# Kernel tuning notes

Measured on AMD Instinct MI355X. Metric: run time of the kernel, lower is better.

Reference implementation:

```python
import jax, jax.numpy as jnp
import numpy as np

EMB_DIM = 1024
NUM_HEADS = 16
HEAD_DIM = EMB_DIM // NUM_HEADS
B, S = 4, 1024


def _split_heads(x):
    # [B, S, E] -> [B, H, S, E/H]
    b, s, e = x.shape
    return x.reshape(b, s, NUM_HEADS, e // NUM_HEADS).transpose(0, 2, 1, 3)


def _merge_heads(x):
    # [B, H, S, D] -> [B, S, H*D]
    b, h, s, d = x.shape
    return x.transpose(0, 2, 1, 3).reshape(b, s, h * d)


def setup_inputs() -> dict:
    key = jax.random.key(0)
    ks = jax.random.split(key, 8)
    w_scale = 0.02
    return {
        "Re": jax.random.normal(ks[0], (B, S, EMB_DIM), jnp.float32),
        "Im": jax.random.normal(ks[1], (B, S, EMB_DIM), jnp.float32),
        "pos_enc": jax.random.normal(ks[2], (B, S, HEAD_DIM), jnp.float32),
        "Wq": jax.random.normal(ks[3], (EMB_DIM, EMB_DIM), jnp.float32) * w_scale,
        "bq": jnp.zeros((EMB_DIM,), jnp.float32),
        "Wk": jax.random.normal(ks[4], (EMB_DIM, EMB_DIM), jnp.float32) * w_scale,
        "bk": jnp.zeros((EMB_DIM,), jnp.float32),
        "Wv": jax.random.normal(ks[5], (EMB_DIM, EMB_DIM), jnp.float32) * w_scale,
        "bv": jnp.zeros((EMB_DIM,), jnp.float32),
        "Wo": jax.random.normal(ks[6], (EMB_DIM, EMB_DIM), jnp.float32) * w_scale,
        "bo": jnp.zeros((EMB_DIM,), jnp.float32),
    }


def reference(Re, Im, pos_enc, Wq, bq, Wk, bk, Wv, bv, Wo, bo):
    # projections + head split
    Q = _split_heads(Re @ Wq + bq)          # [B,H,S,D]
    K = _split_heads(Re @ Wk + bk)          # [B,H,S,D]
    ImH = _split_heads(Im)                  # [B,H,S,D]
    P = pos_enc[:, None, :, :]              # [B,1,S,D] broadcast over heads
    Q = Q + P
    K = K + P
    # real part of (Q + i*Im)(K - i*Im)^T = Q K^T + Im Im^T
    denom = jnp.sqrt(jnp.asarray(EMB_DIM, Q.dtype))  # NOTE: sqrt(emb_dim), as in source
    scores = (jnp.einsum("bhqd,bhkd->bhqk", Q, K)
              + jnp.einsum("bhqd,bhkd->bhqk", ImH, ImH)) / denom
    weights = jax.nn.softmax(scores, axis=-1)
    V = _split_heads(Re @ Wv + bv) + P      # value_pos_enc=True
    out = jnp.einsum("bhqk,bhkd->bhqd", weights, V)
    return _merge_heads(out) @ Wo + bo
```

## Files before the change

kernel.cpp:

```cpp
#include <hip/hip_runtime.h>
#include <hip/hip_bf16.h>
#include <stdint.h>

#define BATCH 4
#define SEQ   1024
#define EMB   1024
#define NHEAD 16
#define HDIM  64
#define MTOT  (BATCH*SEQ)
#define MELEM (MTOT*EMB)

typedef __attribute__((ext_vector_type(8))) short short8;
typedef __attribute__((ext_vector_type(4))) float f32x4;
typedef __attribute__((ext_vector_type(4))) unsigned short us4;

static __device__ __forceinline__ unsigned short f2bf_fast(float f) {
  unsigned u = __builtin_bit_cast(unsigned, f);
  return (unsigned short)((u + 0x8000u) >> 16);
}

static __device__ __forceinline__ void cp16(const void* g, const void* lds_uniform) {
  __builtin_amdgcn_global_load_lds(
      (const __attribute__((address_space(1))) unsigned int*)(uintptr_t)g,
      (__attribute__((address_space(3))) unsigned int*)(unsigned int)(uintptr_t)lds_uniform,
      16, 0, 0);
}

__global__ __launch_bounds__(256) void cvt_bf16(const float* __restrict__ in0,
                                                const float* __restrict__ in1,
                                                short* __restrict__ out0,
                                                short* __restrict__ out1) {
  const float* in  = blockIdx.y ? in1  : in0;
  short*       out = blockIdx.y ? out1 : out0;
  int i = blockIdx.x * 256 + threadIdx.x;
  float4 f = ((const float4*)in)[i];
  unsigned r0 = ((unsigned)f2bf_fast(f.y) << 16) | f2bf_fast(f.x);
  unsigned r1 = ((unsigned)f2bf_fast(f.w) << 16) | f2bf_fast(f.z);
  ((uint2*)out)[i] = make_uint2(r0, r1);
}

__global__ __launch_bounds__(256) void wtrans(const float* __restrict__ W0,
                                              const float* __restrict__ W1,
                                              const float* __restrict__ W2,
                                              const float* __restrict__ W3,
                                              short* __restrict__ WtBase) {
  const int z = blockIdx.z;
  const float* W = (z == 0) ? W0 : (z == 1) ? W1 : (z == 2) ? W2 : W3;
  short* Wt = WtBase + (size_t)z * EMB * EMB;
  __shared__ short tile[32][33];
  int nT = blockIdx.x * 32, kT = blockIdx.y * 32;
  int tx = threadIdx.x, ty = threadIdx.y;
  #pragma unroll
  for (int i = 0; i < 4; ++i)
    tile[ty + 8*i][tx] = (short)f2bf_fast(W[(size_t)(kT + ty + 8*i) * EMB + nT + tx]);
  __syncthreads();
  #pragma unroll
  for (int i = 0; i < 4; ++i)
    Wt[(size_t)(nT + ty + 8*i) * EMB + kT + tx] = tile[tx][ty + 8*i];
}

__global__ __launch_bounds__(256) void gemm_qkv(const short* __restrict__ A,
                                                const short* __restrict__ Wt,
                                                const float* __restrict__ bq,
                                                const float* __restrict__ bk,
                                                const float* __restrict__ bv,
                                                const float* __restrict__ pos,
                                                short* __restrict__ QKbase,
                                                short* __restrict__ vtOut) {
  const int m0 = blockIdx.y * 128, n0 = blockIdx.x * 64;
  const int z = n0 >> 10;
  const float* bias = (z == 0) ? bq : (z == 1 ? bk : bv);

  __shared__ __align__(16) short As[128 * 64];
  __shared__ __align__(16) short Bs[64 * 64];

  const int t = threadIdx.x;
  const int lane = t & 63, w = t >> 6;
  const int wm = w >> 1, wn = w & 1;
  const int quad = lane >> 4, l16 = lane & 15;
  const int lrow8 = lane >> 3, lchunk = lane & 7;
  const int gch = lchunk ^ lrow8;
  const int sw7 = l16 & 7;

  const short* Arow = A  + (size_t)(m0 + w * 32 + lrow8) * EMB + gch * 8;
  const short* Brow = Wt + (size_t)(n0 + w * 16 + lrow8) * EMB + gch * 8;

  f32x4 acc[4][2] = {};

  for (int k0 = 0; k0 < EMB; k0 += 64) {
    #pragma unroll
    for (int s = 0; s < 4; ++s)
      cp16(Arow + (size_t)(s * 8) * EMB + k0, &As[(w * 32 + s * 8) * 64]);
    #pragma unroll
    for (int s = 0; s < 2; ++s)
      cp16(Brow + (size_t)(s * 8) * EMB + k0, &Bs[(w * 16 + s * 8) * 64]);
    __syncthreads();
    #pragma unroll
    for (int ks = 0; ks < 2; ++ks) {
      const int chv = ((ks << 2) + quad) ^ sw7;
      short8 af[4], bfr[2];
      #pragma unroll
      for (int i = 0; i < 4; ++i)
        af[i] = *(const short8*)&As[(wm * 64 + i * 16 + l16) * 64 + chv * 8];
      #pragma unroll
      for (int j = 0; j < 2; ++j)
        bfr[j] = *(const short8*)&Bs[(wn * 32 + j * 16 + l16) * 64 + chv * 8];
      #pragma unroll
      for (int i = 0; i < 4; ++i)
        #pragma unroll
        for (int j = 0; j < 2; ++j)
          acc[i][j] = __builtin_amdgcn_mfma_f32_16x16x32_bf16(af[i], bfr[j], acc[i][j], 0, 0, 0);
    }
    __syncthreads();
  }

  #pragma unroll
  for (int i = 0; i < 4; ++i) {
    int mbase = m0 + wm * 64 + i * 16 + quad * 4;
    #pragma unroll
    for (int j = 0; j < 2; ++j) {
      int n = n0 + wn * 32 + j * 16 + l16;
      int nl = n & 1023;
      float bn = bias[nl];
      int d = nl & (HDIM - 1);
      if (z == 2) {
        int bh = (mbase >> 10) * NHEAD + (nl >> 6);
        int s = mbase & (SEQ - 1);
        us4 pk;
        #pragma unroll
        for (int r = 0; r < 4; ++r) {
          float v = acc[i][j][r] + bn + pos[(size_t)(mbase + r) * HDIM + d];
          pk[r] = f2bf_fast(v);
        }
        *(us4*)&vtOut[((size_t)bh * HDIM + d) * SEQ + s] = pk;
      } else {
        #pragma unroll
        for (int r = 0; r < 4; ++r) {
          int mm = mbase + r;
          float v = acc[i][j][r] + bn + pos[(size_t)mm * HDIM + d];
          QKbase[(size_t)z * MELEM + (size_t)mm * EMB + nl] = (short)f2bf_fast(v);
        }
      }
    }
  }
}

__global__ __launch_bounds__(256) void gemm_wo(const short* __restrict__ A,
                                               const short* __restrict__ Bt,
                                               const float* __restrict__ bias,
                                               float* __restrict__ out) {
  const int m0 = blockIdx.y * 64, n0 = blockIdx.x * 64;

  __shared__ __align__(16) short As[64 * 64];
  __shared__ __align__(16) short Bs[64 * 64];

  const int t = threadIdx.x;
  const int lane = t & 63, w = t >> 6;
  const int wm = w >> 1, wn = w & 1;
  const int quad = lane >> 4, l16 = lane & 15;
  const int lrow8 = lane >> 3, lchunk = lane & 7;
  const int gch = lchunk ^ lrow8;
  const int sw7 = l16 & 7;

  const short* Arow = A  + (size_t)(m0 + w * 16 + lrow8) * EMB + gch * 8;
  const short* Brow = Bt + (size_t)(n0 + w * 16 + lrow8) * EMB + gch * 8;

  f32x4 acc[2][2] = {};

  for (int k0 = 0; k0 < EMB; k0 += 64) {
    #pragma unroll
    for (int s = 0; s < 2; ++s) {
      cp16(Arow + (size_t)(s * 8) * EMB + k0, &As[(w * 16 + s * 8) * 64]);
      cp16(Brow + (size_t)(s * 8) * EMB + k0, &Bs[(w * 16 + s * 8) * 64]);
    }
    __syncthreads();
    #pragma unroll
    for (int ks = 0; ks < 2; ++ks) {
      const int chv = ((ks << 2) + quad) ^ sw7;
      short8 af[2], bfr[2];
      #pragma unroll
      for (int i = 0; i < 2; ++i)
        af[i] = *(const short8*)&As[(wm * 32 + i * 16 + l16) * 64 + chv * 8];
      #pragma unroll
      for (int j = 0; j < 2; ++j)
        bfr[j] = *(const short8*)&Bs[(wn * 32 + j * 16 + l16) * 64 + chv * 8];
      #pragma unroll
      for (int i = 0; i < 2; ++i)
        #pragma unroll
        for (int j = 0; j < 2; ++j)
          acc[i][j] = __builtin_amdgcn_mfma_f32_16x16x32_bf16(af[i], bfr[j], acc[i][j], 0, 0, 0);
    }
    __syncthreads();
  }

  #pragma unroll
  for (int i = 0; i < 2; ++i) {
    int mbase = m0 + wm * 32 + i * 16 + quad * 4;
    #pragma unroll
    for (int j = 0; j < 2; ++j) {
      int n = n0 + wn * 32 + j * 16 + l16;
      float bn = bias[n];
      #pragma unroll
      for (int r = 0; r < 4; ++r)
        out[(size_t)(mbase + r) * EMB + n] = acc[i][j][r] + bn;
    }
  }
}

__global__ __launch_bounds__(256) void attn(const short* __restrict__ Qp,
                                            const short* __restrict__ Kp,
                                            const short* __restrict__ VtG,
                                            const short* __restrict__ Imb,
                                            short* __restrict__ attnA) {
  const int qb = blockIdx.y * 64;
  const int bh = blockIdx.x;
  const int b = bh >> 4, h = bh & 15;
  const int t = threadIdx.x, lane = t & 63, w = t >> 6;
  const int quad = lane >> 4, l16 = lane & 15;
  const int lrow8 = lane >> 3, lchunk = lane & 7;
  const int gch = lchunk ^ lrow8;
  const int sw7 = l16 & 7;

  __shared__ __align__(16) short tiles[3 * 64 * 64];
  __shared__ __align__(16) short Pw[4 * 16 * 64];

  const int q = qb + w * 16 + l16;
  const size_t qoff = ((size_t)(b * SEQ + q)) * EMB + h * HDIM + quad * 8;
  short8 aq[2], aim[2];
  aq[0]  = *(const short8*)&Qp [qoff];
  aq[1]  = *(const short8*)&Qp [qoff + 32];
  aim[0] = *(const short8*)&Imb[qoff];
  aim[1] = *(const short8*)&Imb[qoff + 32];

  float lr[4] = {0.f, 0.f, 0.f, 0.f};
  f32x4 o[4] = {};

  const float SC = 0.03125f * 1.44269504089f;
  const size_t kimBase = ((size_t)b * SEQ) * EMB + h * HDIM + gch * 8;
  const size_t vtBase  = ((size_t)bh * HDIM) * SEQ + gch * 8;

  #pragma unroll
  for (int s = 0; s < 6; ++s) {
    const int I = w * 6 + s;
    const int tz = I >> 3;
    const int row = ((I & 7) * 8) + lrow8;
    const short* g;
    if (tz == 0)      g = Kp  + kimBase + (size_t)row * EMB;
    else if (tz == 1) g = Imb + kimBase + (size_t)row * EMB;
    else              g = VtG + vtBase + (size_t)row * SEQ;
    cp16(g, &tiles[I * 512]);
  }
  __syncthreads();

  for (int kt = 0; kt < 16; ++kt) {
    const int kBaseN = (kt + 1) * 64;

    f32x4 sa[4] = {};
    #pragma unroll
    for (int c = 0; c < 4; ++c) {
      const int rowoff = (c * 16 + l16) * 64;
      #pragma unroll
      for (int st = 0; st < 2; ++st) {
        const int chv = (((st << 2) + quad) ^ sw7) * 8;
        short8 bk = *(const short8*)&tiles[rowoff + chv];
        short8 bi = *(const short8*)&tiles[4096 + rowoff + chv];
        sa[c] = __builtin_amdgcn_mfma_f32_16x16x32_bf16(aq [st], bk, sa[c], 0, 0, 0);
        sa[c] = __builtin_amdgcn_mfma_f32_16x16x32_bf16(aim[st], bi, sa[c], 0, 0, 0);
      }
    }

    __syncthreads();

    if (kt != 15) {
      #pragma unroll
      for (int s = 0; s < 4; ++s) {
        const int I = w * 4 + s;
        const int row = ((I & 7) * 8) + lrow8;
        const short* g = ((I >> 3) ? Imb : Kp) + kimBase + (size_t)(kBaseN + row) * EMB;
        cp16(g, &tiles[I * 512]);
      }
    }

    short* pw = &Pw[w * 1024];
    #pragma unroll
    for (int c = 0; c < 4; ++c) {
      #pragma unroll
      for (int r = 0; r < 4; ++r) {
        float p = __builtin_amdgcn_exp2f(sa[c][r] * SC);
        lr[r] += p;
        const int row = quad * 4 + r;
        const int sch = ((c * 2 + (l16 >> 3)) ^ (row & 7));
        pw[row * 64 + sch * 8 + (l16 & 7)] = (short)f2bf_fast(p);
      }
    }
    short8 ap[2];
    ap[0] = *(const short8*)&pw[l16 * 64 + ((quad       ^ sw7) * 8)];
    ap[1] = *(const short8*)&pw[l16 * 64 + (((4 + quad) ^ sw7) * 8)];

    #pragma unroll
    for (int cd = 0; cd < 4; ++cd) {
      const int rowoff = 8192 + (cd * 16 + l16) * 64;
      #pragma unroll
      for (int st = 0; st < 2; ++st) {
        short8 bv2 = *(const short8*)&tiles[rowoff + (((st << 2) + quad) ^ sw7) * 8];
        o[cd] = __builtin_amdgcn_mfma_f32_16x16x32_bf16(ap[st], bv2, o[cd], 0, 0, 0);
      }
    }

    __syncthreads();

    if (kt != 15) {
      #pragma unroll
      for (int s = 0; s < 2; ++s) {
        const int I = 16 + w * 2 + s;
        const int row = ((I & 7) * 8) + lrow8;
        cp16(VtG + vtBase + (size_t)row * SEQ + kBaseN, &tiles[I * 512]);
      }
    }
  }

  #pragma unroll
  for (int r = 0; r < 4; ++r) {
    #pragma unroll
    for (int msk = 1; msk < 16; msk <<= 1) lr[r] += __shfl_xor(lr[r], msk);
  }
  #pragma unroll
  for (int r = 0; r < 4; ++r) {
    int qq = qb + w * 16 + quad * 4 + r;
    float inv = 1.f / lr[r];
    size_t base = ((size_t)(b * SEQ + qq)) * EMB + h * HDIM;
    #pragma unroll
    for (int cd = 0; cd < 4; ++cd)
      attnA[base + cd * 16 + l16] = (short)f2bf_fast(o[cd][r] * inv);
  }
}

extern "C" void kernel_launch(void* const* d_in, const int* in_sizes, int n_in,
                              void* d_out, int out_size, void* d_ws, size_t ws_size,
                              hipStream_t stream) {
  const float* Re  = (const float*)d_in[0];
  const float* Im  = (const float*)d_in[1];
  const float* pos = (const float*)d_in[2];
  const float* Wq  = (const float*)d_in[3];
  const float* bq  = (const float*)d_in[4];
  const float* Wk  = (const float*)d_in[5];
  const float* bk  = (const float*)d_in[6];
  const float* Wv  = (const float*)d_in[7];
  const float* bv  = (const float*)d_in[8];
  const float* Wo  = (const float*)d_in[9];
  const float* bo  = (const float*)d_in[10];

  short* ws    = (short*)d_ws;
  short* Rebf  = ws;
  short* Imbf  = ws + (size_t)MELEM;
  short* Wt    = ws + (size_t)2 * MELEM;
  short* Qp    = ws + (size_t)3 * MELEM;
  short* Kp    = Qp + (size_t)MELEM;
  short* VtG   = Qp + (size_t)2 * MELEM;
  short* attnA = ws + (size_t)6 * MELEM;

  cvt_bf16<<<dim3(MELEM / 1024, 2), 256, 0, stream>>>(Re, Im, Rebf, Imbf);

  wtrans<<<dim3(32, 32, 4), dim3(32, 8), 0, stream>>>(Wq, Wk, Wv, Wo, Wt);

  gemm_qkv<<<dim3(3 * EMB / 64, MTOT / 128), 256, 0, stream>>>(
      Rebf, Wt, bq, bk, bv, pos, Qp, VtG);

  attn<<<dim3(BATCH * NHEAD, SEQ / 64), 256, 0, stream>>>(
      Qp, Kp, VtG, Imbf, attnA);

  gemm_wo<<<dim3(EMB / 64, MTOT / 64), 256, 0, stream>>>(
      attnA, Wt + 3 * EMB * EMB, bo, (float*)d_out);
}
```

Baseline: 206.1 us.

## Enlarge output tiles in QKV, Wo and attention kernels for more reuse

Doubles the per-block tile in all three compute kernels: the QKV GEMM goes to 128x128, the Wo GEMM to 128x64, and each attention block handles 128 queries with two 16-row groups per wave. Each K/Im/V tile loaded into LDS now feeds twice as many MFMAs, which cuts global and LDS traffic per FLOP. In exchange, accumulator register pressure rises and grids shrink (attention drops to 512 blocks, QKV to 768), which can hurt occupancy and how evenly blocks spread across CUs.

```diff
diff --git a/kernel.cpp b/kernel.cpp
--- a/kernel.cpp
+++ b/kernel.cpp
@@ -67,12 +67,12 @@
                                                 const float* __restrict__ pos,
                                                 short* __restrict__ QKbase,
                                                 short* __restrict__ vtOut) {
-  const int m0 = blockIdx.y * 128, n0 = blockIdx.x * 64;
+  const int m0 = blockIdx.y * 128, n0 = blockIdx.x * 128;
   const int z = n0 >> 10;
   const float* bias = (z == 0) ? bq : (z == 1 ? bk : bv);
 
   __shared__ __align__(16) short As[128 * 64];
-  __shared__ __align__(16) short Bs[64 * 64];
+  __shared__ __align__(16) short Bs[128 * 64];
 
   const int t = threadIdx.x;
   const int lane = t & 63, w = t >> 6;
@@ -83,32 +83,32 @@
   const int sw7 = l16 & 7;
 
   const short* Arow = A  + (size_t)(m0 + w * 32 + lrow8) * EMB + gch * 8;
-  const short* Brow = Wt + (size_t)(n0 + w * 16 + lrow8) * EMB + gch * 8;
-
-  f32x4 acc[4][2] = {};
+  const short* Brow = Wt + (size_t)(n0 + w * 32 + lrow8) * EMB + gch * 8;
+
+  f32x4 acc[4][4] = {};
 
   for (int k0 = 0; k0 < EMB; k0 += 64) {
     #pragma unroll
     for (int s = 0; s < 4; ++s)
       cp16(Arow + (size_t)(s * 8) * EMB + k0, &As[(w * 32 + s * 8) * 64]);
     #pragma unroll
-    for (int s = 0; s < 2; ++s)
-      cp16(Brow + (size_t)(s * 8) * EMB + k0, &Bs[(w * 16 + s * 8) * 64]);
+    for (int s = 0; s < 4; ++s)
+      cp16(Brow + (size_t)(s * 8) * EMB + k0, &Bs[(w * 32 + s * 8) * 64]);
     __syncthreads();
     #pragma unroll
     for (int ks = 0; ks < 2; ++ks) {
       const int chv = ((ks << 2) + quad) ^ sw7;
-      short8 af[4], bfr[2];
+      short8 af[4], bfr[4];
       #pragma unroll
       for (int i = 0; i < 4; ++i)
         af[i] = *(const short8*)&As[(wm * 64 + i * 16 + l16) * 64 + chv * 8];
       #pragma unroll
-      for (int j = 0; j < 2; ++j)
-        bfr[j] = *(const short8*)&Bs[(wn * 32 + j * 16 + l16) * 64 + chv * 8];
+      for (int j = 0; j < 4; ++j)
+        bfr[j] = *(const short8*)&Bs[(wn * 64 + j * 16 + l16) * 64 + chv * 8];
       #pragma unroll
       for (int i = 0; i < 4; ++i)
         #pragma unroll
-        for (int j = 0; j < 2; ++j)
+        for (int j = 0; j < 4; ++j)
           acc[i][j] = __builtin_amdgcn_mfma_f32_16x16x32_bf16(af[i], bfr[j], acc[i][j], 0, 0, 0);
     }
     __syncthreads();
@@ -118,8 +118,8 @@
   for (int i = 0; i < 4; ++i) {
     int mbase = m0 + wm * 64 + i * 16 + quad * 4;
     #pragma unroll
-    for (int j = 0; j < 2; ++j) {
-      int n = n0 + wn * 32 + j * 16 + l16;
+    for (int j = 0; j < 4; ++j) {
+      int n = n0 + wn * 64 + j * 16 + l16;
       int nl = n & 1023;
       float bn = bias[nl];
       int d = nl & (HDIM - 1);
@@ -149,9 +149,9 @@
                                                const short* __restrict__ Bt,
                                                const float* __restrict__ bias,
                                                float* __restrict__ out) {
-  const int m0 = blockIdx.y * 64, n0 = blockIdx.x * 64;
-
-  __shared__ __align__(16) short As[64 * 64];
+  const int m0 = blockIdx.y * 128, n0 = blockIdx.x * 64;
+
+  __shared__ __align__(16) short As[128 * 64];
   __shared__ __align__(16) short Bs[64 * 64];
 
   const int t = threadIdx.x;
@@ -162,30 +162,31 @@
   const int gch = lchunk ^ lrow8;
   const int sw7 = l16 & 7;
 
-  const short* Arow = A  + (size_t)(m0 + w * 16 + lrow8) * EMB + gch * 8;
+  const short* Arow = A  + (size_t)(m0 + w * 32 + lrow8) * EMB + gch * 8;
   const short* Brow = Bt + (size_t)(n0 + w * 16 + lrow8) * EMB + gch * 8;
 
-  f32x4 acc[2][2] = {};
+  f32x4 acc[4][2] = {};
 
   for (int k0 = 0; k0 < EMB; k0 += 64) {
     #pragma unroll
-    for (int s = 0; s < 2; ++s) {
-      cp16(Arow + (size_t)(s * 8) * EMB + k0, &As[(w * 16 + s * 8) * 64]);
+    for (int s = 0; s < 4; ++s)
+      cp16(Arow + (size_t)(s * 8) * EMB + k0, &As[(w * 32 + s * 8) * 64]);
+    #pragma unroll
+    for (int s = 0; s < 2; ++s)
       cp16(Brow + (size_t)(s * 8) * EMB + k0, &Bs[(w * 16 + s * 8) * 64]);
-    }
     __syncthreads();
     #pragma unroll
     for (int ks = 0; ks < 2; ++ks) {
       const int chv = ((ks << 2) + quad) ^ sw7;
-      short8 af[2], bfr[2];
-      #pragma unroll
-      for (int i = 0; i < 2; ++i)
-        af[i] = *(const short8*)&As[(wm * 32 + i * 16 + l16) * 64 + chv * 8];
+      short8 af[4], bfr[2];
+      #pragma unroll
+      for (int i = 0; i < 4; ++i)
+        af[i] = *(const short8*)&As[(wm * 64 + i * 16 + l16) * 64 + chv * 8];
       #pragma unroll
       for (int j = 0; j < 2; ++j)
         bfr[j] = *(const short8*)&Bs[(wn * 32 + j * 16 + l16) * 64 + chv * 8];
       #pragma unroll
-      for (int i = 0; i < 2; ++i)
+      for (int i = 0; i < 4; ++i)
         #pragma unroll
         for (int j = 0; j < 2; ++j)
           acc[i][j] = __builtin_amdgcn_mfma_f32_16x16x32_bf16(af[i], bfr[j], acc[i][j], 0, 0, 0);
@@ -194,8 +195,8 @@
   }
 
   #pragma unroll
-  for (int i = 0; i < 2; ++i) {
-    int mbase = m0 + wm * 32 + i * 16 + quad * 4;
+  for (int i = 0; i < 4; ++i) {
+    int mbase = m0 + wm * 64 + i * 16 + quad * 4;
     #pragma unroll
     for (int j = 0; j < 2; ++j) {
       int n = n0 + wn * 32 + j * 16 + l16;
@@ -212,7 +213,7 @@
                                             const short* __restrict__ VtG,
                                             const short* __restrict__ Imb,
                                             short* __restrict__ attnA) {
-  const int qb = blockIdx.y * 64;
+  const int qb = blockIdx.y * 128;
   const int bh = blockIdx.x;
   const int b = bh >> 4, h = bh & 15;
   const int t = threadIdx.x, lane = t & 63, w = t >> 6;
@@ -222,18 +223,21 @@
   const int sw7 = l16 & 7;
 
   __shared__ __align__(16) short tiles[3 * 64 * 64];
-  __shared__ __align__(16) short Pw[4 * 16 * 64];
-
-  const int q = qb + w * 16 + l16;
-  const size_t qoff = ((size_t)(b * SEQ + q)) * EMB + h * HDIM + quad * 8;
-  short8 aq[2], aim[2];
-  aq[0]  = *(const short8*)&Qp [qoff];
-  aq[1]  = *(const short8*)&Qp [qoff + 32];
-  aim[0] = *(const short8*)&Imb[qoff];
-  aim[1] = *(const short8*)&Imb[qoff + 32];
-
-  float lr[4] = {0.f, 0.f, 0.f, 0.f};
-  f32x4 o[4] = {};
+  __shared__ __align__(16) short Pw[4 * 32 * 64];
+
+  short8 aq[2][2], aim[2][2];
+  #pragma unroll
+  for (int g = 0; g < 2; ++g) {
+    const int q = qb + w * 32 + g * 16 + l16;
+    const size_t qoff = ((size_t)(b * SEQ + q)) * EMB + h * HDIM + quad * 8;
+    aq[g][0]  = *(const short8*)&Qp [qoff];
+    aq[g][1]  = *(const short8*)&Qp [qoff + 32];
+    aim[g][0] = *(const short8*)&Imb[qoff];
+    aim[g][1] = *(const short8*)&Imb[qoff + 32];
+  }
+
+  float lr[2][4] = {};
+  f32x4 o[2][4] = {};
 
   const float SC = 0.03125f * 1.44269504089f;
   const size_t kimBase = ((size_t)b * SEQ) * EMB + h * HDIM + gch * 8;
@@ -255,7 +259,7 @@
   for (int kt = 0; kt < 16; ++kt) {
     const int kBaseN = (kt + 1) * 64;
 
-    f32x4 sa[4] = {};
+    f32x4 sa[2][4] = {};
     #pragma unroll
     for (int c = 0; c < 4; ++c) {
       const int rowoff = (c * 16 + l16) * 64;
@@ -264,8 +268,11 @@
         const int chv = (((st << 2) + quad) ^ sw7) * 8;
         short8 bk = *(const short8*)&tiles[rowoff + chv];
         short8 bi = *(const short8*)&tiles[4096 + rowoff + chv];
-        sa[c] = __builtin_amdgcn_mfma_f32_16x16x32_bf16(aq [st], bk, sa[c], 0, 0, 0);
-        sa[c] = __builtin_amdgcn_mfma_f32_16x16x32_bf16(aim[st], bi, sa[c], 0, 0, 0);
+        #pragma unroll
+        for (int g = 0; g < 2; ++g) {
+          sa[g][c] = __builtin_amdgcn_mfma_f32_16x16x32_bf16(aq [g][st], bk, sa[g][c], 0, 0, 0);
+          sa[g][c] = __builtin_amdgcn_mfma_f32_16x16x32_bf16(aim[g][st], bi, sa[g][c], 0, 0, 0);
+        }
       }
     }
 
@@ -281,21 +288,27 @@
       }
     }
 
-    short* pw = &Pw[w * 1024];
-    #pragma unroll
-    for (int c = 0; c < 4; ++c) {
-      #pragma unroll
-      for (int r = 0; r < 4; ++r) {
-        float p = __builtin_amdgcn_exp2f(sa[c][r] * SC);
-        lr[r] += p;
-        const int row = quad * 4 + r;
-        const int sch = ((c * 2 + (l16 >> 3)) ^ (row & 7));
-        pw[row * 64 + sch * 8 + (l16 & 7)] = (short)f2bf_fast(p);
-      }
-    }
-    short8 ap[2];
-    ap[0] = *(const short8*)&pw[l16 * 64 + ((quad       ^ sw7) * 8)];
-    ap[1] = *(const short8*)&pw[l16 * 64 + (((4 + quad) ^ sw7) * 8)];
+    short* pw = &Pw[w * 2048];
+    #pragma unroll
+    for (int g = 0; g < 2; ++g) {
+      #pragma unroll
+      for (int c = 0; c < 4; ++c) {
+        #pragma unroll
+        for (int r = 0; r < 4; ++r) {
+          float p = __builtin_amdgcn_exp2f(sa[g][c][r] * SC);
+          lr[g][r] += p;
+          const int row = quad * 4 + r;
+          const int sch = ((c * 2 + (l16 >> 3)) ^ (row & 7));
+          pw[(g * 16 + row) * 64 + sch * 8 + (l16 & 7)] = (short)f2bf_fast(p);
+        }
+      }
+    }
+    short8 ap[2][2];
+    #pragma unroll
+    for (int g = 0; g < 2; ++g) {
+      ap[g][0] = *(const short8*)&pw[(g * 16 + l16) * 64 + ((quad       ^ sw7) * 8)];
+      ap[g][1] = *(const short8*)&pw[(g * 16 + l16) * 64 + (((4 + quad) ^ sw7) * 8)];
+    }
 
     #pragma unroll
     for (int cd = 0; cd < 4; ++cd) {
@@ -303,7 +316,9 @@
       #pragma unroll
       for (int st = 0; st < 2; ++st) {
         short8 bv2 = *(const short8*)&tiles[rowoff + (((st << 2) + quad) ^ sw7) * 8];
-        o[cd] = __builtin_amdgcn_mfma_f32_16x16x32_bf16(ap[st], bv2, o[cd], 0, 0, 0);
+        #pragma unroll
+        for (int g = 0; g < 2; ++g)
+          o[g][cd] = __builtin_amdgcn_mfma_f32_16x16x32_bf16(ap[g][st], bv2, o[g][cd], 0, 0, 0);
       }
     }
 
@@ -320,18 +335,23 @@
   }
 
   #pragma unroll
-  for (int r = 0; r < 4; ++r) {
-    #pragma unroll
-    for (int msk = 1; msk < 16; msk <<= 1) lr[r] += __shfl_xor(lr[r], msk);
-  }
-  #pragma unroll
-  for (int r = 0; r < 4; ++r) {
-    int qq = qb + w * 16 + quad * 4 + r;
-    float inv = 1.f / lr[r];
-    size_t base = ((size_t)(b * SEQ + qq)) * EMB + h * HDIM;
-    #pragma unroll
-    for (int cd = 0; cd < 4; ++cd)
-      attnA[base + cd * 16 + l16] = (short)f2bf_fast(o[cd][r] * inv);
+  for (int g = 0; g < 2; ++g)
+    #pragma unroll
+    for (int r = 0; r < 4; ++r) {
+      #pragma unroll
+      for (int msk = 1; msk < 16; msk <<= 1) lr[g][r] += __shfl_xor(lr[g][r], msk);
+    }
+  #pragma unroll
+  for (int g = 0; g < 2; ++g) {
+    #pragma unroll
+    for (int r = 0; r < 4; ++r) {
+      int qq = qb + w * 32 + g * 16 + quad * 4 + r;
+      float inv = 1.f / lr[g][r];
+      size_t base = ((size_t)(b * SEQ + qq)) * EMB + h * HDIM;
+      #pragma unroll
+      for (int cd = 0; cd < 4; ++cd)
+        attnA[base + cd * 16 + l16] = (short)f2bf_fast(o[g][cd][r] * inv);
+    }
   }
 }
 
@@ -363,12 +383,12 @@
 
   wtrans<<<dim3(32, 32, 4), dim3(32, 8), 0, stream>>>(Wq, Wk, Wv, Wo, Wt);
 
-  gemm_qkv<<<dim3(3 * EMB / 64, MTOT / 128), 256, 0, stream>>>(
+  gemm_qkv<<<dim3(3 * EMB / 128, MTOT / 128), 256, 0, stream>>>(
       Rebf, Wt, bq, bk, bv, pos, Qp, VtG);
 
-  attn<<<dim3(BATCH * NHEAD, SEQ / 64), 256, 0, stream>>>(
+  attn<<<dim3(BATCH * NHEAD, SEQ / 128), 256, 0, stream>>>(
       Qp, Kp, VtG, Imbf, attnA);
 
-  gemm_wo<<<dim3(EMB / 64, MTOT / 64), 256, 0, stream>>>(
+  gemm_wo<<<dim3(EMB / 64, MTOT / 128), 256, 0, stream>>>(
       attnA, Wt + 3 * EMB * EMB, bo, (float*)d_out);
 }
```

Result: slower. 211.2 us (+2.5%).

## Use 32x32 MFMA in attention with register-resident P via permlane32 swap

Applied to the files above, without the earlier changes.

Rewrites the attention kernel to use 32x32x16 bf16 MFMA, computing S transposed (K as A operand) so each wave handles 32 queries and each block 128 queries. The probabilities are converted to bf16 with packed cvt and rearranged in registers with permlane32_swap instead of a round trip through LDS, which removes the Pw buffer and its stores and loads. Doubling queries per block halves the K/Im/V tile loads per query but halves the grid size, which lowers occupancy and parallelism.

```diff
diff --git a/kernel.cpp b/kernel.cpp
--- a/kernel.cpp
+++ b/kernel.cpp
@@ -12,11 +12,20 @@
 
 typedef __attribute__((ext_vector_type(8))) short short8;
 typedef __attribute__((ext_vector_type(4))) float f32x4;
+typedef __attribute__((ext_vector_type(16))) float f32x16;
 typedef __attribute__((ext_vector_type(4))) unsigned short us4;
+typedef __attribute__((ext_vector_type(2))) unsigned int u32x2;
+typedef __attribute__((ext_vector_type(4))) unsigned int u32x4;
 
 static __device__ __forceinline__ unsigned short f2bf_fast(float f) {
   unsigned u = __builtin_bit_cast(unsigned, f);
   return (unsigned short)((u + 0x8000u) >> 16);
+}
+
+static __device__ __forceinline__ unsigned cvt_pk_bf16(float lo, float hi) {
+  unsigned r;
+  asm("v_cvt_pk_bf16_f32 %0, %1, %2" : "=v"(r) : "v"(lo), "v"(hi));
+  return r;
 }
 
 static __device__ __forceinline__ void cp16(const void* g, const void* lds_uniform) {
@@ -212,28 +221,28 @@
                                             const short* __restrict__ VtG,
                                             const short* __restrict__ Imb,
                                             short* __restrict__ attnA) {
-  const int qb = blockIdx.y * 64;
+  const int qb = blockIdx.y * 128;
   const int bh = blockIdx.x;
   const int b = bh >> 4, h = bh & 15;
   const int t = threadIdx.x, lane = t & 63, w = t >> 6;
-  const int quad = lane >> 4, l16 = lane & 15;
+  const int c31 = lane & 31;
+  const int hi  = lane >> 5;
   const int lrow8 = lane >> 3, lchunk = lane & 7;
   const int gch = lchunk ^ lrow8;
-  const int sw7 = l16 & 7;
 
   __shared__ __align__(16) short tiles[3 * 64 * 64];
-  __shared__ __align__(16) short Pw[4 * 16 * 64];
-
-  const int q = qb + w * 16 + l16;
-  const size_t qoff = ((size_t)(b * SEQ + q)) * EMB + h * HDIM + quad * 8;
-  short8 aq[2], aim[2];
-  aq[0]  = *(const short8*)&Qp [qoff];
-  aq[1]  = *(const short8*)&Qp [qoff + 32];
-  aim[0] = *(const short8*)&Imb[qoff];
-  aim[1] = *(const short8*)&Imb[qoff + 32];
-
-  float lr[4] = {0.f, 0.f, 0.f, 0.f};
-  f32x4 o[4] = {};
+
+  const int qrow = qb + w * 32 + c31;
+  const size_t qbase = ((size_t)(b * SEQ + qrow)) * EMB + h * HDIM + hi * 8;
+  short8 bq_[4], bim[4];
+  #pragma unroll
+  for (int ks = 0; ks < 4; ++ks) {
+    bq_[ks] = *(const short8*)&Qp [qbase + ks * 16];
+    bim[ks] = *(const short8*)&Imb[qbase + ks * 16];
+  }
+
+  float lrA = 0.f, lrB = 0.f;
+  f32x16 o0 = {}, o1 = {};
 
   const float SC = 0.03125f * 1.44269504089f;
   const size_t kimBase = ((size_t)b * SEQ) * EMB + h * HDIM + gch * 8;
@@ -252,21 +261,24 @@
   }
   __syncthreads();
 
+  const int swz = c31 & 7;
+
   for (int kt = 0; kt < 16; ++kt) {
     const int kBaseN = (kt + 1) * 64;
 
-    f32x4 sa[4] = {};
-    #pragma unroll
-    for (int c = 0; c < 4; ++c) {
-      const int rowoff = (c * 16 + l16) * 64;
-      #pragma unroll
-      for (int st = 0; st < 2; ++st) {
-        const int chv = (((st << 2) + quad) ^ sw7) * 8;
-        short8 bk = *(const short8*)&tiles[rowoff + chv];
-        short8 bi = *(const short8*)&tiles[4096 + rowoff + chv];
-        sa[c] = __builtin_amdgcn_mfma_f32_16x16x32_bf16(aq [st], bk, sa[c], 0, 0, 0);
-        sa[c] = __builtin_amdgcn_mfma_f32_16x16x32_bf16(aim[st], bi, sa[c], 0, 0, 0);
-      }
+    f32x16 s0 = {}, s1 = {};
+    #pragma unroll
+    for (int ks = 0; ks < 4; ++ks) {
+      const int ch = ((ks * 2 + hi) ^ swz) * 8;
+      const int r0off = c31 * 64 + ch, r1off = (32 + c31) * 64 + ch;
+      short8 k0 = *(const short8*)&tiles[r0off];
+      short8 k1 = *(const short8*)&tiles[r1off];
+      short8 i0 = *(const short8*)&tiles[4096 + r0off];
+      short8 i1 = *(const short8*)&tiles[4096 + r1off];
+      s0 = __builtin_amdgcn_mfma_f32_32x32x16_bf16(k0, bq_[ks], s0, 0, 0, 0);
+      s1 = __builtin_amdgcn_mfma_f32_32x32x16_bf16(k1, bq_[ks], s1, 0, 0, 0);
+      s0 = __builtin_amdgcn_mfma_f32_32x32x16_bf16(i0, bim[ks], s0, 0, 0, 0);
+      s1 = __builtin_amdgcn_mfma_f32_32x32x16_bf16(i1, bim[ks], s1, 0, 0, 0);
     }
 
     __syncthreads();
@@ -281,30 +293,43 @@
       }
     }
 
-    short* pw = &Pw[w * 1024];
-    #pragma unroll
-    for (int c = 0; c < 4; ++c) {
-      #pragma unroll
-      for (int r = 0; r < 4; ++r) {
-        float p = __builtin_amdgcn_exp2f(sa[c][r] * SC);
-        lr[r] += p;
-        const int row = quad * 4 + r;
-        const int sch = ((c * 2 + (l16 >> 3)) ^ (row & 7));
-        pw[row * 64 + sch * 8 + (l16 & 7)] = (short)f2bf_fast(p);
-      }
-    }
-    short8 ap[2];
-    ap[0] = *(const short8*)&pw[l16 * 64 + ((quad       ^ sw7) * 8)];
-    ap[1] = *(const short8*)&pw[l16 * 64 + (((4 + quad) ^ sw7) * 8)];
-
-    #pragma unroll
-    for (int cd = 0; cd < 4; ++cd) {
-      const int rowoff = 8192 + (cd * 16 + l16) * 64;
-      #pragma unroll
-      for (int st = 0; st < 2; ++st) {
-        short8 bv2 = *(const short8*)&tiles[rowoff + (((st << 2) + quad) ^ sw7) * 8];
-        o[cd] = __builtin_amdgcn_mfma_f32_16x16x32_bf16(ap[st], bv2, o[cd], 0, 0, 0);
-      }
+    float p0[16], p1[16];
+    #pragma unroll
+    for (int r = 0; r < 16; ++r) {
+      p0[r] = __builtin_amdgcn_exp2f(s0[r] * SC);
+      p1[r] = __builtin_amdgcn_exp2f(s1[r] * SC);
+      lrA += p0[r];
+      lrB += p1[r];
+    }
+
+    short8 ap[4];
+    #pragma unroll
+    for (int half = 0; half < 2; ++half) {
+      {
+        u32x2 sA = __builtin_amdgcn_permlane32_swap(
+            cvt_pk_bf16(p0[half*8+0], p0[half*8+1]), cvt_pk_bf16(p0[half*8+4], p0[half*8+5]), false, false);
+        u32x2 sB = __builtin_amdgcn_permlane32_swap(
+            cvt_pk_bf16(p0[half*8+2], p0[half*8+3]), cvt_pk_bf16(p0[half*8+6], p0[half*8+7]), false, false);
+        u32x4 wv = {sA[0], sB[0], sA[1], sB[1]};
+        ap[half] = __builtin_bit_cast(short8, wv);
+      }
+      {
+        u32x2 sA = __builtin_amdgcn_permlane32_swap(
+            cvt_pk_bf16(p1[half*8+0], p1[half*8+1]), cvt_pk_bf16(p1[half*8+4], p1[half*8+5]), false, false);
+        u32x2 sB = __builtin_amdgcn_permlane32_swap(
+            cvt_pk_bf16(p1[half*8+2], p1[half*8+3]), cvt_pk_bf16(p1[half*8+6], p1[half*8+7]), false, false);
+        u32x4 wv = {sA[0], sB[0], sA[1], sB[1]};
+        ap[2 + half] = __builtin_bit_cast(short8, wv);
+      }
+    }
+
+    #pragma unroll
+    for (int ks = 0; ks < 4; ++ks) {
+      const int ch = ((ks * 2 + hi) ^ swz) * 8;
+      short8 v0 = *(const short8*)&tiles[8192 + c31 * 64 + ch];
+      short8 v1 = *(const short8*)&tiles[8192 + (32 + c31) * 64 + ch];
+      o0 = __builtin_amdgcn_mfma_f32_32x32x16_bf16(ap[ks], v0, o0, 0, 0, 0);
+      o1 = __builtin_amdgcn_mfma_f32_32x32x16_bf16(ap[ks], v1, o1, 0, 0, 0);
     }
 
     __syncthreads();
@@ -319,19 +344,17 @@
     }
   }
 
-  #pragma unroll
-  for (int r = 0; r < 4; ++r) {
-    #pragma unroll
-    for (int msk = 1; msk < 16; msk <<= 1) lr[r] += __shfl_xor(lr[r], msk);
-  }
-  #pragma unroll
-  for (int r = 0; r < 4; ++r) {
-    int qq = qb + w * 16 + quad * 4 + r;
-    float inv = 1.f / lr[r];
-    size_t base = ((size_t)(b * SEQ + qq)) * EMB + h * HDIM;
-    #pragma unroll
-    for (int cd = 0; cd < 4; ++cd)
-      attnA[base + cd * 16 + l16] = (short)f2bf_fast(o[cd][r] * inv);
+  float lr = lrA + lrB;
+  lr += __shfl_xor(lr, 32);
+  float inv = 1.f / lr;
+
+  #pragma unroll
+  for (int r = 0; r < 16; ++r) {
+    const int qr = (r & 3) + 8 * (r >> 2) + 4 * hi;
+    const float invr = __shfl(inv, qr);
+    const size_t base = ((size_t)(b * SEQ + qb + w * 32 + qr)) * EMB + h * HDIM + c31;
+    attnA[base]      = (short)f2bf_fast(o0[r] * invr);
+    attnA[base + 32] = (short)f2bf_fast(o1[r] * invr);
   }
 }
 
@@ -366,7 +389,7 @@
   gemm_qkv<<<dim3(3 * EMB / 64, MTOT / 128), 256, 0, stream>>>(
       Rebf, Wt, bq, bk, bv, pos, Qp, VtG);
 
-  attn<<<dim3(BATCH * NHEAD, SEQ / 64), 256, 0, stream>>>(
+  attn<<<dim3(BATCH * NHEAD, SEQ / 128), 256, 0, stream>>>(
       Qp, Kp, VtG, Imbf, attnA);
 
   gemm_wo<<<dim3(EMB / 64, MTOT / 64), 256, 0, stream>>>(
```

New measurement: 193.7 us. 6.0% less time.
